# Kernel optimization log

Measured on AMD Instinct MI355X. Metric: run time of the kernel, lower is better.

## Reference

```python
import jax, jax.numpy as jnp
import numpy as np

B, N = 16, 131072
C_MID, C_OUT = 128, 16


def setup_inputs() -> dict:
    key = jax.random.key(0)
    k1, k2, k3, k4 = jax.random.split(key, 4)
    # points in roughly [-0.5, 0.5] so cube indexing covers the grids
    x = jax.random.uniform(k1, (B, N, 3), dtype=jnp.float32) - 0.5
    W1 = jax.random.normal(k2, (C_MID, 3), dtype=jnp.float32) * 0.1
    b1 = jnp.zeros((C_MID,), jnp.float32)
    W2 = jax.random.normal(k3, (C_OUT, C_MID), dtype=jnp.float32) * 0.1
    b2 = jnp.zeros((C_OUT,), jnp.float32)
    # fixed per-batch permutations (deterministic stand-in for torch.randperm)
    perm = jnp.stack([jax.random.permutation(jax.random.fold_in(k4, i), N)
                      for i in range(B)]).astype(jnp.int32)
    return {"x": x, "W1": W1, "b1": b1, "W2": W2, "b2": b2, "perm": perm}


def point_to_cell(pts, feat, W, H, D):
    # pts float [B,N,3] already clamped to [0, dim-1]; cast like torch LongTensor
    idx = pts.astype(jnp.int32)
    flat = (idx[..., 0] * H + idx[..., 1]) * D + idx[..., 2]  # [B,N]
    Bb, Nn, C = feat.shape

    def scatter_one(fi, fe):
        grid = jnp.zeros((W * H * D, C), feat.dtype)
        return grid.at[fi].set(fe)

    cell = jax.vmap(scatter_one)(flat, feat)           # [B, WHD, C]
    return cell.transpose(0, 2, 1).reshape(Bb, C, W, H, D)


def reference(x, W1, b1, W2, b2, perm):
    # PointNetfeatLocal: 1x1 Conv1d stack == per-point MLP 3 -> 128 -> 16
    h = jnp.maximum(jnp.einsum('bnc,hc->bnh', x, W1) + b1, 0.0)
    feat = jnp.einsum('bnh,oh->bno', h, W2) + b2       # [B,N,16]
    # shuffle_points_feat: per-batch permutation gather
    xs = jnp.take_along_axis(x, perm[..., None], axis=1)
    fs = jnp.take_along_axis(feat, perm[..., None], axis=1)
    # batch_grid_pooling32 / 64
    cube32 = jnp.clip(xs * 32.0 + 16.5, 0.0, 31.0)
    cube64 = jnp.clip(xs * 64.0 + 32.5, 0.0, 63.0)
    feat_cell32 = point_to_cell(cube32, fs, 32, 32, 32)  # [B,16,32,32,32]
    feat_cell64 = point_to_cell(cube64, fs, 64, 64, 64)  # [B,16,64,64,64]
    return feat_cell32, feat_cell64
```

## Files before the change

### kernel.cpp

```cpp
#include <hip/hip_runtime.h>

namespace {
constexpr int kB = 16;
constexpr int kN = 131072;
constexpr int kNLog = 17;
constexpr int kCMid = 128;
constexpr int kCOut = 16;
constexpr int kCells32Log = 15;
constexpr int kCells64Log = 18;
constexpr int kCells32 = 1 << kCells32Log;
constexpr int kCells64 = 1 << kCells64Log;
constexpr long kOut32Elems = (long)kB * kCOut * kCells32;
}

union F32U { float f; unsigned int u; };

__device__ inline unsigned int packbf2(float lo, float hi) {
    F32U a; a.f = lo;
    F32U b; b.f = hi;
    unsigned int ra = (a.u + 0x7FFFu + ((a.u >> 16) & 1u)) >> 16;
    unsigned int rb = (b.u + 0x7FFFu + ((b.u >> 16) & 1u)) >> 16;
    return (rb << 16) | (ra & 0xFFFFu);
}

__device__ inline float bf_lo(unsigned int p) { F32U v; v.u = p << 16; return v.f; }
__device__ inline float bf_hi(unsigned int p) { F32U v; v.u = p & 0xFFFF0000u; return v.f; }

__global__ __launch_bounds__(256) void pack_weights(
    const float* __restrict__ W1, const float* __restrict__ b1,
    const float* __restrict__ W2,
    float* __restrict__ W1p, float* __restrict__ W2t)
{
    const int t = threadIdx.x;
    for (int k = t; k < kCMid; k += 256) {
        W1p[k * 4 + 0] = W1[k * 3 + 0];
        W1p[k * 4 + 1] = W1[k * 3 + 1];
        W1p[k * 4 + 2] = W1[k * 3 + 2];
        W1p[k * 4 + 3] = b1[k];
    }
    for (int idx = t; idx < kCOut * kCMid; idx += 256) {
        const int c = idx >> 7;
        const int k = idx & 127;
        W2t[k * kCOut + c] = W2[idx];
    }
}

__global__ __launch_bounds__(256) void fused_scatter_mlp(
    const float* __restrict__ x,
    const int* __restrict__ perm,
    const float* __restrict__ W1p, const float* __restrict__ W2t,
    const float* __restrict__ b2,
    unsigned int* __restrict__ win32, unsigned int* __restrict__ win64,
    uint4* __restrict__ feat)
{
    const long gid = (long)blockIdx.x * 256 + threadIdx.x;
    const int b = (int)(gid >> kNLog);
    const int i = (int)(gid & (kN - 1));
    const int j = perm[gid];

    const float* xp = x + ((long)b * kN + j) * 3;
    const float v0 = xp[0], v1 = xp[1], v2 = xp[2];

    const int ix32 = (int)fminf(fmaxf(__fadd_rn(__fmul_rn(v0, 32.0f), 16.5f), 0.0f), 31.0f);
    const int iy32 = (int)fminf(fmaxf(__fadd_rn(__fmul_rn(v1, 32.0f), 16.5f), 0.0f), 31.0f);
    const int iz32 = (int)fminf(fmaxf(__fadd_rn(__fmul_rn(v2, 32.0f), 16.5f), 0.0f), 31.0f);
    const int ix64 = (int)fminf(fmaxf(__fadd_rn(__fmul_rn(v0, 64.0f), 32.5f), 0.0f), 63.0f);
    const int iy64 = (int)fminf(fmaxf(__fadd_rn(__fmul_rn(v1, 64.0f), 32.5f), 0.0f), 63.0f);
    const int iz64 = (int)fminf(fmaxf(__fadd_rn(__fmul_rn(v2, 64.0f), 32.5f), 0.0f), 63.0f);

    const unsigned int pri = (unsigned int)(i + 1);
    atomicMax(&win32[b * kCells32 + (ix32 * 32 + iy32) * 32 + iz32], pri);
    atomicMax(&win64[b * kCells64 + (ix64 * 64 + iy64) * 64 + iz64], pri);

    float acc[kCOut];
    #pragma unroll
    for (int c = 0; c < kCOut; ++c) acc[c] = 0.0f;

    const float4* __restrict__ w1v = (const float4*)W1p;
    const float4* __restrict__ w2v = (const float4*)W2t;

    #pragma unroll 4
    for (int k = 0; k < kCMid; ++k) {
        const float4 w1 = w1v[k];
        const float h = fmaxf(fmaf(w1.x, v0, fmaf(w1.y, v1, fmaf(w1.z, v2, w1.w))), 0.0f);
        #pragma unroll
        for (int q = 0; q < 4; ++q) {
            const float4 wq = w2v[k * 4 + q];
            acc[4 * q + 0] = fmaf(wq.x, h, acc[4 * q + 0]);
            acc[4 * q + 1] = fmaf(wq.y, h, acc[4 * q + 1]);
            acc[4 * q + 2] = fmaf(wq.z, h, acc[4 * q + 2]);
            acc[4 * q + 3] = fmaf(wq.w, h, acc[4 * q + 3]);
        }
    }

    const float4 bq0 = ((const float4*)b2)[0];
    const float4 bq1 = ((const float4*)b2)[1];
    const float4 bq2 = ((const float4*)b2)[2];
    const float4 bq3 = ((const float4*)b2)[3];

    uint4 f0, f1;
    f0.x = packbf2(acc[0]  + bq0.x, acc[1]  + bq0.y);
    f0.y = packbf2(acc[2]  + bq0.z, acc[3]  + bq0.w);
    f0.z = packbf2(acc[4]  + bq1.x, acc[5]  + bq1.y);
    f0.w = packbf2(acc[6]  + bq1.z, acc[7]  + bq1.w);
    f1.x = packbf2(acc[8]  + bq2.x, acc[9]  + bq2.y);
    f1.y = packbf2(acc[10] + bq2.z, acc[11] + bq2.w);
    f1.z = packbf2(acc[12] + bq3.x, acc[13] + bq3.y);
    f1.w = packbf2(acc[14] + bq3.z, acc[15] + bq3.w);
    feat[gid * 2 + 0] = f0;
    feat[gid * 2 + 1] = f1;
}

template <int CLOG>
__global__ __launch_bounds__(256) void gather_cells(
    const unsigned int* __restrict__ win,
    const uint4* __restrict__ feat,
    float* __restrict__ out)
{
    constexpr int cells = 1 << CLOG;
    const long gid = (long)blockIdx.x * 256 + threadIdx.x;
    const int b = (int)(gid >> CLOG);
    const int cell = (int)(gid & (cells - 1));
    const unsigned int w = win[gid];

    float v[kCOut];
    #pragma unroll
    for (int c = 0; c < kCOut; ++c) v[c] = 0.0f;

    if (w != 0u) {
        const long pidx = ((long)b << kNLog) + (long)(w - 1u);
        const uint4 f0 = feat[pidx * 2 + 0];
        const uint4 f1 = feat[pidx * 2 + 1];
        v[0]  = bf_lo(f0.x); v[1]  = bf_hi(f0.x);
        v[2]  = bf_lo(f0.y); v[3]  = bf_hi(f0.y);
        v[4]  = bf_lo(f0.z); v[5]  = bf_hi(f0.z);
        v[6]  = bf_lo(f0.w); v[7]  = bf_hi(f0.w);
        v[8]  = bf_lo(f1.x); v[9]  = bf_hi(f1.x);
        v[10] = bf_lo(f1.y); v[11] = bf_hi(f1.y);
        v[12] = bf_lo(f1.z); v[13] = bf_hi(f1.z);
        v[14] = bf_lo(f1.w); v[15] = bf_hi(f1.w);
    }

    float* op = out + (((long)b * kCOut) << CLOG) + cell;
    #pragma unroll
    for (int c = 0; c < kCOut; ++c) op[(long)c << CLOG] = v[c];
}

extern "C" void kernel_launch(void* const* d_in, const int* in_sizes, int n_in,
                              void* d_out, int out_size, void* d_ws, size_t ws_size,
                              hipStream_t stream)
{
    const float* x  = (const float*)d_in[0];
    const float* W1 = (const float*)d_in[1];
    const float* b1 = (const float*)d_in[2];
    const float* W2 = (const float*)d_in[3];
    const float* b2 = (const float*)d_in[4];
    const int* perm = (const int*)d_in[5];

    float* out32 = (float*)d_out;
    float* out64 = out32 + kOut32Elems;

    float* W1p = (float*)d_ws;
    float* W2t = W1p + kCMid * 4;
    unsigned int* win32 = (unsigned int*)((char*)d_ws + 16384);
    unsigned int* win64 = win32 + (size_t)kB * kCells32;
    const size_t winnerBytes = (size_t)kB * (kCells32 + kCells64) * sizeof(unsigned int);
    uint4* feat = (uint4*)((char*)win32 + winnerBytes);

    hipMemsetAsync(win32, 0, winnerBytes, stream);
    pack_weights<<<1, 256, 0, stream>>>(W1, b1, W2, W1p, W2t);

    const int nPtsBlocks = (int)(((long)kB * kN) / 256);
    const int n32Blocks  = (int)(((long)kB * kCells32) / 256);
    const int n64Blocks  = (int)(((long)kB * kCells64) / 256);
    dim3 blk(256);

    fused_scatter_mlp<<<nPtsBlocks, blk, 0, stream>>>(
        x, perm, W1p, W2t, b2, win32, win64, feat);
    gather_cells<kCells32Log><<<n32Blocks, blk, 0, stream>>>(win32, feat, out32);
    gather_cells<kCells64Log><<<n64Blocks, blk, 0, stream>>>(win64, feat, out64);
}
```

Measured before the change: 294.5 us.

## Invert permutation to read points coalesced and store original index in 64-bit winner token

Adds a kernel that builds the inverse permutation, so the fused MLP/scatter kernel reads x in natural order (coalesced) rather than through the perm gather. Features are written in unpermuted order. The winner atomics become 64-bit tokens holding the shuffled priority in the high half and the original point index in the low half, so the gather stage can find the feature directly. This doubles winner-buffer size and adds an extra scattered-write pass to build the inverse, and the memset is replaced by a custom zero kernel.

```diff
diff --git a/kernel.cpp b/kernel.cpp
--- a/kernel.cpp
+++ b/kernel.cpp
@@ -11,22 +11,35 @@
 constexpr int kCells32 = 1 << kCells32Log;
 constexpr int kCells64 = 1 << kCells64Log;
 constexpr long kOut32Elems = (long)kB * kCOut * kCells32;
-}
-
-union F32U { float f; unsigned int u; };
+constexpr long kWinU4 = (long)kB * (kCells32 + kCells64) / 2;
+}
 
 __device__ inline unsigned int packbf2(float lo, float hi) {
-    F32U a; a.f = lo;
-    F32U b; b.f = hi;
-    unsigned int ra = (a.u + 0x7FFFu + ((a.u >> 16) & 1u)) >> 16;
-    unsigned int rb = (b.u + 0x7FFFu + ((b.u >> 16) & 1u)) >> 16;
-    return (rb << 16) | (ra & 0xFFFFu);
-}
-
-__device__ inline float bf_lo(unsigned int p) { F32U v; v.u = p << 16; return v.f; }
-__device__ inline float bf_hi(unsigned int p) { F32U v; v.u = p & 0xFFFF0000u; return v.f; }
-
-__global__ __launch_bounds__(256) void pack_weights(
+    unsigned int a = __float_as_uint(lo);
+    unsigned int b = __float_as_uint(hi);
+    a = (a + 0x7FFFu + ((a >> 16) & 1u)) >> 16;
+    b = (b + 0x7FFFu + ((b >> 16) & 1u)) & 0xFFFF0000u;
+    return b | a;
+}
+__device__ inline float bf_lo(unsigned int p) { return __uint_as_float(p << 16); }
+__device__ inline float bf_hi(unsigned int p) { return __uint_as_float(p & 0xFFFF0000u); }
+
+__global__ __launch_bounds__(256) void k_zero(uint4* __restrict__ p)
+{
+    const long stride = (long)gridDim.x * 256;
+    for (long idx = (long)blockIdx.x * 256 + threadIdx.x; idx < kWinU4; idx += stride)
+        p[idx] = make_uint4(0u, 0u, 0u, 0u);
+}
+
+__global__ __launch_bounds__(256) void k_inv(
+    const int* __restrict__ perm, int* __restrict__ inv)
+{
+    const long gid = (long)blockIdx.x * 256 + threadIdx.x;
+    const long bbase = gid & ~(long)(kN - 1);
+    inv[bbase + perm[gid]] = (int)(gid & (kN - 1));
+}
+
+__global__ __launch_bounds__(256) void k_pack(
     const float* __restrict__ W1, const float* __restrict__ b1,
     const float* __restrict__ W2,
     float* __restrict__ W1p, float* __restrict__ W2t)
@@ -45,21 +58,23 @@
     }
 }
 
-__global__ __launch_bounds__(256) void fused_scatter_mlp(
+__global__ __launch_bounds__(256) void k_fused(
     const float* __restrict__ x,
-    const int* __restrict__ perm,
+    const int* __restrict__ inv,
     const float* __restrict__ W1p, const float* __restrict__ W2t,
     const float* __restrict__ b2,
-    unsigned int* __restrict__ win32, unsigned int* __restrict__ win64,
+    unsigned long long* __restrict__ win32,
+    unsigned long long* __restrict__ win64,
     uint4* __restrict__ feat)
 {
     const long gid = (long)blockIdx.x * 256 + threadIdx.x;
     const int b = (int)(gid >> kNLog);
-    const int i = (int)(gid & (kN - 1));
-    const int j = perm[gid];
-
-    const float* xp = x + ((long)b * kN + j) * 3;
-    const float v0 = xp[0], v1 = xp[1], v2 = xp[2];
+    const int j = (int)(gid & (kN - 1));
+
+    const float v0 = x[gid * 3 + 0];
+    const float v1 = x[gid * 3 + 1];
+    const float v2 = x[gid * 3 + 2];
+    const unsigned int pri = (unsigned int)(inv[gid] + 1);
 
     const int ix32 = (int)fminf(fmaxf(__fadd_rn(__fmul_rn(v0, 32.0f), 16.5f), 0.0f), 31.0f);
     const int iy32 = (int)fminf(fmaxf(__fadd_rn(__fmul_rn(v1, 32.0f), 16.5f), 0.0f), 31.0f);
@@ -68,9 +83,10 @@
     const int iy64 = (int)fminf(fmaxf(__fadd_rn(__fmul_rn(v1, 64.0f), 32.5f), 0.0f), 63.0f);
     const int iz64 = (int)fminf(fmaxf(__fadd_rn(__fmul_rn(v2, 64.0f), 32.5f), 0.0f), 63.0f);
 
-    const unsigned int pri = (unsigned int)(i + 1);
-    atomicMax(&win32[b * kCells32 + (ix32 * 32 + iy32) * 32 + iz32], pri);
-    atomicMax(&win64[b * kCells64 + (ix64 * 64 + iy64) * 64 + iz64], pri);
+    const unsigned long long tok =
+        ((unsigned long long)pri << 32) | (unsigned int)j;
+    atomicMax(&win32[b * kCells32 + (ix32 * 32 + iy32) * 32 + iz32], tok);
+    atomicMax(&win64[b * kCells64 + (ix64 * 64 + iy64) * 64 + iz64], tok);
 
     float acc[kCOut];
     #pragma unroll
@@ -98,22 +114,22 @@
     const float4 bq2 = ((const float4*)b2)[2];
     const float4 bq3 = ((const float4*)b2)[3];
 
-    uint4 f0, f1;
-    f0.x = packbf2(acc[0]  + bq0.x, acc[1]  + bq0.y);
-    f0.y = packbf2(acc[2]  + bq0.z, acc[3]  + bq0.w);
-    f0.z = packbf2(acc[4]  + bq1.x, acc[5]  + bq1.y);
-    f0.w = packbf2(acc[6]  + bq1.z, acc[7]  + bq1.w);
-    f1.x = packbf2(acc[8]  + bq2.x, acc[9]  + bq2.y);
-    f1.y = packbf2(acc[10] + bq2.z, acc[11] + bq2.w);
-    f1.z = packbf2(acc[12] + bq3.x, acc[13] + bq3.y);
-    f1.w = packbf2(acc[14] + bq3.z, acc[15] + bq3.w);
-    feat[gid * 2 + 0] = f0;
-    feat[gid * 2 + 1] = f1;
+    uint4 f;
+    f.x = packbf2(acc[0]  + bq0.x, acc[1]  + bq0.y);
+    f.y = packbf2(acc[2]  + bq0.z, acc[3]  + bq0.w);
+    f.z = packbf2(acc[4]  + bq1.x, acc[5]  + bq1.y);
+    f.w = packbf2(acc[6]  + bq1.z, acc[7]  + bq1.w);
+    feat[gid * 2 + 0] = f;
+    f.x = packbf2(acc[8]  + bq2.x, acc[9]  + bq2.y);
+    f.y = packbf2(acc[10] + bq2.z, acc[11] + bq2.w);
+    f.z = packbf2(acc[12] + bq3.x, acc[13] + bq3.y);
+    f.w = packbf2(acc[14] + bq3.z, acc[15] + bq3.w);
+    feat[gid * 2 + 1] = f;
 }
 
 template <int CLOG>
-__global__ __launch_bounds__(256) void gather_cells(
-    const unsigned int* __restrict__ win,
+__global__ __launch_bounds__(256) void k_gather(
+    const unsigned long long* __restrict__ win,
     const uint4* __restrict__ feat,
     float* __restrict__ out)
 {
@@ -121,14 +137,15 @@
     const long gid = (long)blockIdx.x * 256 + threadIdx.x;
     const int b = (int)(gid >> CLOG);
     const int cell = (int)(gid & (cells - 1));
-    const unsigned int w = win[gid];
+    const unsigned long long w = win[gid];
 
     float v[kCOut];
     #pragma unroll
     for (int c = 0; c < kCOut; ++c) v[c] = 0.0f;
 
-    if (w != 0u) {
-        const long pidx = ((long)b << kNLog) + (long)(w - 1u);
+    if (w != 0ull) {
+        const int j = (int)(w & 0xFFFFFFFFull);
+        const long pidx = ((long)b << kNLog) + j;
         const uint4 f0 = feat[pidx * 2 + 0];
         const uint4 f1 = feat[pidx * 2 + 1];
         v[0]  = bf_lo(f0.x); v[1]  = bf_hi(f0.x);
@@ -162,21 +179,24 @@
 
     float* W1p = (float*)d_ws;
     float* W2t = W1p + kCMid * 4;
-    unsigned int* win32 = (unsigned int*)((char*)d_ws + 16384);
-    unsigned int* win64 = win32 + (size_t)kB * kCells32;
-    const size_t winnerBytes = (size_t)kB * (kCells32 + kCells64) * sizeof(unsigned int);
-    uint4* feat = (uint4*)((char*)win32 + winnerBytes);
-
-    hipMemsetAsync(win32, 0, winnerBytes, stream);
-    pack_weights<<<1, 256, 0, stream>>>(W1, b1, W2, W1p, W2t);
+    unsigned long long* win32 = (unsigned long long*)((char*)d_ws + 16384);
+    unsigned long long* win64 = win32 + (size_t)kB * kCells32;
+    const size_t winBytes = (size_t)kB * (kCells32 + kCells64) * sizeof(unsigned long long);
+    int* inv = (int*)((char*)win32 + winBytes);
+    uint4* feat = (uint4*)(inv + (size_t)kB * kN);
 
     const int nPtsBlocks = (int)(((long)kB * kN) / 256);
     const int n32Blocks  = (int)(((long)kB * kCells32) / 256);
     const int n64Blocks  = (int)(((long)kB * kCells64) / 256);
     dim3 blk(256);
 
-    fused_scatter_mlp<<<nPtsBlocks, blk, 0, stream>>>(
-        x, perm, W1p, W2t, b2, win32, win64, feat);
-    gather_cells<kCells32Log><<<n32Blocks, blk, 0, stream>>>(win32, feat, out32);
-    gather_cells<kCells64Log><<<n64Blocks, blk, 0, stream>>>(win64, feat, out64);
-}
+    k_zero<<<2048, blk, 0, stream>>>((uint4*)win32);
+    k_inv<<<nPtsBlocks, blk, 0, stream>>>(perm, inv);
+    k_pack<<<1, 256, 0, stream>>>(W1, b1, W2, W1p, W2t);
+
+    k_fused<<<nPtsBlocks, blk, 0, stream>>>(
+        x, inv, W1p, W2t, b2, win32, win64, feat);
+
+    k_gather<kCells32Log><<<n32Blocks, blk, 0, stream>>>(win32, feat, out32);
+    k_gather<kCells64Log><<<n64Blocks, blk, 0, stream>>>(win64, feat, out64);
+}
```

After: 307.4 us. 1.04x slower.
